# Performance work log

Measured on AMD Instinct MI355X. Metric: run time of the kernel, lower is better.

Reference implementation:

```python
import jax, jax.numpy as jnp
import numpy as np

B, S, L, D = 16, 24, 128, 768
A, T = 8, 8
VOCAB = 100


def setup_inputs() -> dict:
    key = jax.random.key(0)
    k1, k2, k3, k4, k5 = jax.random.split(key, 5)
    return {
        "sentence_embeddings": jax.random.normal(k1, (B, S, L, D), dtype=jnp.float32),
        "sentence_attention_masks": jnp.ones((B, S, L), dtype=jnp.int32),
        "sentence_ids": jax.random.randint(k2, (B, S, L), 0, VOCAB, dtype=jnp.int32),
        "predicate_ids": jax.random.randint(k3, (B, S, A, T), 0, VOCAB, dtype=jnp.int32),
        "arg0_ids": jax.random.randint(k4, (B, S, A, T), 0, VOCAB, dtype=jnp.int32),
        "arg1_ids": jax.random.randint(k5, (B, S, A, T), 0, VOCAB, dtype=jnp.int32),
    }


def _mean_pool(emb, masks):
    # emb: [B,S,L,D], masks: [B,S,L] -> [B,S,D]
    m = masks.astype(emb.dtype)
    summed = jnp.einsum("bsld,bsl->bsd", emb, m)
    counts = jnp.clip(jnp.sum(m, axis=-1, keepdims=True), 1, None)
    return summed / counts


def _arg_embedding(arg_ids, sentence_ids, emb):
    # arg_ids: [B,S,A,T] int, sentence_ids: [B,S,L] int, emb: [B,S,L,D]
    # For each arg token (id != 0), mean-pool sentence positions with matching id.
    # Original loop overwrites per token, so the result is from the LAST nonzero
    # token that has at least one match; zeros if none.
    match = (sentence_ids[:, :, None, None, :] == arg_ids[..., None]) & (
        arg_ids[..., None] != 0
    )  # [B,S,A,T,L]
    m = match.astype(emb.dtype)
    cnt = jnp.sum(m, axis=-1)  # [B,S,A,T]
    avg = jnp.einsum("bsatl,bsld->bsatd", m, emb) / jnp.maximum(cnt, 1.0)[..., None]
    valid = cnt > 0  # nonzero token AND has matches
    t_idx = jnp.arange(arg_ids.shape[-1])
    last = jnp.max(jnp.where(valid, t_idx, -1), axis=-1)  # [B,S,A]
    has_any = last >= 0
    gat = jnp.take_along_axis(
        avg, jnp.maximum(last, 0)[..., None, None], axis=3
    ).squeeze(3)  # [B,S,A,D]
    return jnp.where(has_any[..., None], gat, jnp.zeros((), emb.dtype))


def reference(sentence_embeddings, sentence_attention_masks, sentence_ids,
              predicate_ids, arg0_ids, arg1_ids):
    sentence_embeddings_avg = _mean_pool(sentence_embeddings, sentence_attention_masks)
    predicate_embeddings = _arg_embedding(predicate_ids, sentence_ids, sentence_embeddings)
    arg0_embeddings = _arg_embedding(arg0_ids, sentence_ids, sentence_embeddings)
    arg1_embeddings = _arg_embedding(arg1_ids, sentence_ids, sentence_embeddings)
    return (sentence_embeddings_avg, predicate_embeddings, arg0_embeddings, arg1_embeddings)
```

## Files before the change

### kernel.cpp

```cpp
#include <hip/hip_runtime.h>
#include <cstdint>
#include <cstddef>

#define B_ 16
#define S_ 24
#define L_ 128
#define D_ 768
#define A_ 8
#define T_ 8
#define NSLOT 24
#define HALF_D 384
#define THREADS 192
#define QC 96
#define CHUNK 8

__global__ void __launch_bounds__(THREADS)
srl_kernel(const float* __restrict__ emb,
           const int* __restrict__ masks,
           const int* __restrict__ sids,
           const int* __restrict__ pred,
           const int* __restrict__ arg0,
           const int* __restrict__ arg1,
           float* __restrict__ out)
{
    const int blk  = blockIdx.x;
    const int bs   = blk >> 1;
    const int half = blk & 1;
    const int tid  = threadIdx.x;
    const int r    = tid / QC;
    const int c    = tid % QC;

    __shared__ int          sid_sh[L_];
    __shared__ float        mval_sh[L_];
    __shared__ float        inv_mask_cnt;
    __shared__ int          id_st[NSLOT][T_];
    __shared__ int          cnt_st[NSLOT][T_];
    __shared__ int          chosen_id[NSLOT];
    __shared__ float        inv_cnt[NSLOT];
    __shared__ unsigned int lmask[L_];
    __shared__ float        slot_acc[NSLOT][HALF_D];
    __shared__ float        pool_sh[QC][4];

    if (tid < L_) {
        sid_sh[tid]  = sids[bs * L_ + tid];
        mval_sh[tid] = (float)masks[bs * L_ + tid];
    }
    __syncthreads();

    {
        const int s24 = tid >> 3;
        const int t   = tid & 7;
        const int g   = s24 >> 3;
        const int a   = s24 & 7;
        const int* argp = (g == 0) ? pred : (g == 1) ? arg0 : arg1;
        const int id = argp[((bs * A_) + a) * T_ + t];
        int cnt = 0;
        if (id != 0) {
            #pragma unroll 8
            for (int l = 0; l < L_; ++l) cnt += (sid_sh[l] == id) ? 1 : 0;
        }
        id_st[s24][t]  = id;
        cnt_st[s24][t] = cnt;
    }

    {
        float* p = &slot_acc[0][0];
        for (int i = tid; i < NSLOT * HALF_D; i += THREADS) p[i] = 0.0f;
    }
    if (tid == 0) {
        float cm = 0.0f;
        for (int l = 0; l < L_; ++l) cm += mval_sh[l];
        inv_mask_cnt = 1.0f / fmaxf(cm, 1.0f);
    }
    __syncthreads();

    if (tid < NSLOT) {
        int cid = -1;
        int ccnt = 0;
        for (int t = T_ - 1; t >= 0; --t) {
            if (cnt_st[tid][t] > 0) { cid = id_st[tid][t]; ccnt = cnt_st[tid][t]; break; }
        }
        chosen_id[tid] = cid;
        inv_cnt[tid]   = (ccnt > 0) ? (1.0f / (float)ccnt) : 0.0f;
    }
    __syncthreads();

    if (tid < L_) {
        const int s = sid_sh[tid];
        unsigned int m = 0;
        #pragma unroll
        for (int k = 0; k < NSLOT; ++k)
            m |= (unsigned int)(chosen_id[k] == s) << k;
        lmask[tid] = m;
    }
    __syncthreads();

    const float* rp = emb + (size_t)bs * (L_ * D_) + (size_t)r * D_
                    + half * HALF_D + 4 * c;
    float4 p4 = make_float4(0.f, 0.f, 0.f, 0.f);
    for (int i0 = 0; i0 < L_ / 2; i0 += CHUNK) {
        float4 v[CHUNK];
        #pragma unroll
        for (int j = 0; j < CHUNK; ++j)
            v[j] = *(const float4*)(rp + (size_t)(i0 + j) * (2 * D_));
        #pragma unroll
        for (int j = 0; j < CHUNK; ++j) {
            const int l = r + 2 * (i0 + j);
            const float mk = mval_sh[l];
            p4.x = fmaf(v[j].x, mk, p4.x);
            p4.y = fmaf(v[j].y, mk, p4.y);
            p4.z = fmaf(v[j].z, mk, p4.z);
            p4.w = fmaf(v[j].w, mk, p4.w);
            unsigned int m = lmask[l];
            while (m) {
                const int s24 = __ffs(m) - 1;
                m &= m - 1;
                float* ap = &slot_acc[s24][4 * c];
                atomicAdd(ap + 0, v[j].x);
                atomicAdd(ap + 1, v[j].y);
                atomicAdd(ap + 2, v[j].z);
                atomicAdd(ap + 3, v[j].w);
            }
        }
    }

    if (r == 1) {
        pool_sh[c][0] = p4.x; pool_sh[c][1] = p4.y;
        pool_sh[c][2] = p4.z; pool_sh[c][3] = p4.w;
    }
    __syncthreads();

    const size_t out0_sz = (size_t)B_ * S_ * D_;
    const size_t arg_sz  = (size_t)B_ * S_ * A_ * D_;
    const int d0 = half * HALF_D + 4 * c;

    if (r == 0) {
        float4 o;
        o.x = (p4.x + pool_sh[c][0]) * inv_mask_cnt;
        o.y = (p4.y + pool_sh[c][1]) * inv_mask_cnt;
        o.z = (p4.z + pool_sh[c][2]) * inv_mask_cnt;
        o.w = (p4.w + pool_sh[c][3]) * inv_mask_cnt;
        *(float4*)(out + (size_t)bs * D_ + d0) = o;
    }
    #pragma unroll
    for (int si = 0; si < NSLOT / 2; ++si) {
        const int s24 = r * (NSLOT / 2) + si;
        const int g = s24 >> 3;
        const int a = s24 & 7;
        const float ic = inv_cnt[s24];
        const float* ap = &slot_acc[s24][4 * c];
        float4 o;
        o.x = ap[0] * ic; o.y = ap[1] * ic;
        o.z = ap[2] * ic; o.w = ap[3] * ic;
        float* dst = out + out0_sz + (size_t)g * arg_sz
                   + ((size_t)(bs * A_ + a)) * D_ + d0;
        *(float4*)dst = o;
    }
}

extern "C" void kernel_launch(void* const* d_in, const int* in_sizes, int n_in,
                              void* d_out, int out_size, void* d_ws, size_t ws_size,
                              hipStream_t stream) {
    const float* emb = (const float*)d_in[0];
    const int* masks = (const int*)d_in[1];
    const int* sids  = (const int*)d_in[2];
    const int* pred  = (const int*)d_in[3];
    const int* a0    = (const int*)d_in[4];
    const int* a1    = (const int*)d_in[5];
    float* out = (float*)d_out;

    srl_kernel<<<dim3(2 * B_ * S_), dim3(THREADS), 0, stream>>>(
        emb, masks, sids, pred, a0, a1, out);
}
```

Baseline: 273.4 us.

## Split pooling and per-slot argument gathers into separate block roles

```diff
diff --git a/kernel.cpp b/kernel.cpp
--- a/kernel.cpp
+++ b/kernel.cpp
@@ -13,147 +13,141 @@
 #define THREADS 192
 #define QC 96
 #define CHUNK 8
+#define POOL_BLOCKS (2 * B_ * S_)
+#define ARG_BLOCKS  (NSLOT * B_ * S_)
 
-__global__ void __launch_bounds__(THREADS)
-srl_kernel(const float* __restrict__ emb,
-           const int* __restrict__ masks,
-           const int* __restrict__ sids,
-           const int* __restrict__ pred,
-           const int* __restrict__ arg0,
-           const int* __restrict__ arg1,
-           float* __restrict__ out)
+__global__ void __launch_bounds__(THREADS, 4)
+srl_fused(const float* __restrict__ emb,
+          const int* __restrict__ masks,
+          const int* __restrict__ sids,
+          const int* __restrict__ pred,
+          const int* __restrict__ arg0,
+          const int* __restrict__ arg1,
+          float* __restrict__ out)
 {
-    const int blk  = blockIdx.x;
-    const int bs   = blk >> 1;
-    const int half = blk & 1;
-    const int tid  = threadIdx.x;
-    const int r    = tid / QC;
-    const int c    = tid % QC;
+    const int tid = threadIdx.x;
+    const size_t out0_sz = (size_t)B_ * S_ * D_;
+    const size_t arg_sz  = (size_t)B_ * S_ * A_ * D_;
 
-    __shared__ int          sid_sh[L_];
-    __shared__ float        mval_sh[L_];
-    __shared__ float        inv_mask_cnt;
-    __shared__ int          id_st[NSLOT][T_];
-    __shared__ int          cnt_st[NSLOT][T_];
-    __shared__ int          chosen_id[NSLOT];
-    __shared__ float        inv_cnt[NSLOT];
-    __shared__ unsigned int lmask[L_];
-    __shared__ float        slot_acc[NSLOT][HALF_D];
-    __shared__ float        pool_sh[QC][4];
+    if (blockIdx.x < POOL_BLOCKS) {
+        const int blk  = blockIdx.x;
+        const int bs   = blk >> 1;
+        const int half = blk & 1;
+        const int r    = tid / QC;
+        const int c    = tid % QC;
 
-    if (tid < L_) {
-        sid_sh[tid]  = sids[bs * L_ + tid];
-        mval_sh[tid] = (float)masks[bs * L_ + tid];
-    }
-    __syncthreads();
+        __shared__ float mval_sh[L_];
+        __shared__ float pool_sh[QC][4];
+        __shared__ float inv_sh;
 
-    {
-        const int s24 = tid >> 3;
-        const int t   = tid & 7;
-        const int g   = s24 >> 3;
-        const int a   = s24 & 7;
-        const int* argp = (g == 0) ? pred : (g == 1) ? arg0 : arg1;
-        const int id = argp[((bs * A_) + a) * T_ + t];
-        int cnt = 0;
-        if (id != 0) {
-            #pragma unroll 8
-            for (int l = 0; l < L_; ++l) cnt += (sid_sh[l] == id) ? 1 : 0;
+        if (tid < L_) mval_sh[tid] = (float)masks[bs * L_ + tid];
+        __syncthreads();
+
+        if (tid < 64) {
+            float v = mval_sh[tid] + mval_sh[tid + 64];
+            #pragma unroll
+            for (int off = 32; off; off >>= 1) v += __shfl_down(v, off, 64);
+            if (tid == 0) inv_sh = 1.0f / fmaxf(v, 1.0f);
         }
-        id_st[s24][t]  = id;
-        cnt_st[s24][t] = cnt;
-    }
 
-    {
-        float* p = &slot_acc[0][0];
-        for (int i = tid; i < NSLOT * HALF_D; i += THREADS) p[i] = 0.0f;
-    }
-    if (tid == 0) {
-        float cm = 0.0f;
-        for (int l = 0; l < L_; ++l) cm += mval_sh[l];
-        inv_mask_cnt = 1.0f / fmaxf(cm, 1.0f);
-    }
-    __syncthreads();
-
-    if (tid < NSLOT) {
-        int cid = -1;
-        int ccnt = 0;
-        for (int t = T_ - 1; t >= 0; --t) {
-            if (cnt_st[tid][t] > 0) { cid = id_st[tid][t]; ccnt = cnt_st[tid][t]; break; }
-        }
-        chosen_id[tid] = cid;
-        inv_cnt[tid]   = (ccnt > 0) ? (1.0f / (float)ccnt) : 0.0f;
-    }
-    __syncthreads();
-
-    if (tid < L_) {
-        const int s = sid_sh[tid];
-        unsigned int m = 0;
-        #pragma unroll
-        for (int k = 0; k < NSLOT; ++k)
-            m |= (unsigned int)(chosen_id[k] == s) << k;
-        lmask[tid] = m;
-    }
-    __syncthreads();
-
-    const float* rp = emb + (size_t)bs * (L_ * D_) + (size_t)r * D_
-                    + half * HALF_D + 4 * c;
-    float4 p4 = make_float4(0.f, 0.f, 0.f, 0.f);
-    for (int i0 = 0; i0 < L_ / 2; i0 += CHUNK) {
-        float4 v[CHUNK];
-        #pragma unroll
-        for (int j = 0; j < CHUNK; ++j)
-            v[j] = *(const float4*)(rp + (size_t)(i0 + j) * (2 * D_));
-        #pragma unroll
-        for (int j = 0; j < CHUNK; ++j) {
-            const int l = r + 2 * (i0 + j);
-            const float mk = mval_sh[l];
-            p4.x = fmaf(v[j].x, mk, p4.x);
-            p4.y = fmaf(v[j].y, mk, p4.y);
-            p4.z = fmaf(v[j].z, mk, p4.z);
-            p4.w = fmaf(v[j].w, mk, p4.w);
-            unsigned int m = lmask[l];
-            while (m) {
-                const int s24 = __ffs(m) - 1;
-                m &= m - 1;
-                float* ap = &slot_acc[s24][4 * c];
-                atomicAdd(ap + 0, v[j].x);
-                atomicAdd(ap + 1, v[j].y);
-                atomicAdd(ap + 2, v[j].z);
-                atomicAdd(ap + 3, v[j].w);
+        const float* rp = emb + (size_t)bs * (L_ * D_) + (size_t)r * D_
+                        + half * HALF_D + 4 * c;
+        float4 p = make_float4(0.f, 0.f, 0.f, 0.f);
+        for (int i0 = 0; i0 < L_ / 2; i0 += CHUNK) {
+            float4 v[CHUNK];
+            #pragma unroll
+            for (int j = 0; j < CHUNK; ++j)
+                v[j] = *(const float4*)(rp + (size_t)(i0 + j) * (2 * D_));
+            #pragma unroll
+            for (int j = 0; j < CHUNK; ++j) {
+                const float mk = mval_sh[r + 2 * (i0 + j)];
+                p.x = fmaf(v[j].x, mk, p.x);
+                p.y = fmaf(v[j].y, mk, p.y);
+                p.z = fmaf(v[j].z, mk, p.z);
+                p.w = fmaf(v[j].w, mk, p.w);
             }
         }
-    }
+        if (r == 1) {
+            pool_sh[c][0] = p.x; pool_sh[c][1] = p.y;
+            pool_sh[c][2] = p.z; pool_sh[c][3] = p.w;
+        }
+        __syncthreads();
+        if (r == 0) {
+            const float iv = inv_sh;
+            float4 o;
+            o.x = (p.x + pool_sh[c][0]) * iv;
+            o.y = (p.y + pool_sh[c][1]) * iv;
+            o.z = (p.z + pool_sh[c][2]) * iv;
+            o.w = (p.w + pool_sh[c][3]) * iv;
+            *(float4*)(out + (size_t)bs * D_ + half * HALF_D + 4 * c) = o;
+        }
+    } else {
+        const int task = blockIdx.x - POOL_BLOCKS;
+        const int bs   = task / NSLOT;
+        const int slot = task - bs * NSLOT;
+        const int g    = slot >> 3;
+        const int a    = slot & 7;
 
-    if (r == 1) {
-        pool_sh[c][0] = p4.x; pool_sh[c][1] = p4.y;
-        pool_sh[c][2] = p4.z; pool_sh[c][3] = p4.w;
-    }
-    __syncthreads();
+        __shared__ int   sid_sh[L_];
+        __shared__ int   tok_id[T_];
+        __shared__ int   tok_cnt[T_];
+        __shared__ int   cid_sh;
+        __shared__ float inv_sh2;
+        __shared__ int   mlist[L_];
+        __shared__ int   mcount;
 
-    const size_t out0_sz = (size_t)B_ * S_ * D_;
-    const size_t arg_sz  = (size_t)B_ * S_ * A_ * D_;
-    const int d0 = half * HALF_D + 4 * c;
+        if (tid < L_) sid_sh[tid] = sids[bs * L_ + tid];
+        if (tid < T_) {
+            const int* ap = (g == 0) ? pred : (g == 1) ? arg0 : arg1;
+            tok_id[tid]  = ap[(bs * A_ + a) * T_ + tid];
+            tok_cnt[tid] = 0;
+        }
+        if (tid == 0) mcount = 0;
+        __syncthreads();
 
-    if (r == 0) {
+        for (int idx = tid; idx < T_ * L_; idx += THREADS) {
+            const int t  = idx >> 7;
+            const int l  = idx & (L_ - 1);
+            const int id = tok_id[t];
+            if (id != 0 && sid_sh[l] == id) atomicAdd(&tok_cnt[t], 1);
+        }
+        __syncthreads();
+
+        if (tid == 0) {
+            int cid = -1; float iv = 0.f;
+            for (int t = T_ - 1; t >= 0; --t)
+                if (tok_cnt[t] > 0) { cid = tok_id[t]; iv = 1.0f / (float)tok_cnt[t]; break; }
+            cid_sh = cid; inv_sh2 = iv;
+        }
+        __syncthreads();
+
+        if (tid < L_ && sid_sh[tid] == cid_sh) {
+            const int pos = atomicAdd(&mcount, 1);
+            mlist[pos] = tid;
+        }
+        __syncthreads();
+        if (tid == 0) {
+            const int n = mcount;
+            for (int i = 1; i < n; ++i) {
+                const int key = mlist[i]; int j = i - 1;
+                while (j >= 0 && mlist[j] > key) { mlist[j + 1] = mlist[j]; --j; }
+                mlist[j + 1] = key;
+            }
+        }
+        __syncthreads();
+
+        const int n = mcount;
+        float4 acc = make_float4(0.f, 0.f, 0.f, 0.f);
+        const float* base = emb + (size_t)bs * (L_ * D_) + 4 * tid;
+        for (int i = 0; i < n; ++i) {
+            const float4 v = *(const float4*)(base + (size_t)mlist[i] * D_);
+            acc.x += v.x; acc.y += v.y; acc.z += v.z; acc.w += v.w;
+        }
+        const float iv = inv_sh2;
         float4 o;
-        o.x = (p4.x + pool_sh[c][0]) * inv_mask_cnt;
-        o.y = (p4.y + pool_sh[c][1]) * inv_mask_cnt;
-        o.z = (p4.z + pool_sh[c][2]) * inv_mask_cnt;
-        o.w = (p4.w + pool_sh[c][3]) * inv_mask_cnt;
-        *(float4*)(out + (size_t)bs * D_ + d0) = o;
-    }
-    #pragma unroll
-    for (int si = 0; si < NSLOT / 2; ++si) {
-        const int s24 = r * (NSLOT / 2) + si;
-        const int g = s24 >> 3;
-        const int a = s24 & 7;
-        const float ic = inv_cnt[s24];
-        const float* ap = &slot_acc[s24][4 * c];
-        float4 o;
-        o.x = ap[0] * ic; o.y = ap[1] * ic;
-        o.z = ap[2] * ic; o.w = ap[3] * ic;
+        o.x = acc.x * iv; o.y = acc.y * iv; o.z = acc.z * iv; o.w = acc.w * iv;
         float* dst = out + out0_sz + (size_t)g * arg_sz
-                   + ((size_t)(bs * A_ + a)) * D_ + d0;
+                   + (size_t)(bs * A_ + a) * D_ + 4 * tid;
         *(float4*)dst = o;
     }
 }
@@ -169,6 +163,6 @@
     const int* a1    = (const int*)d_in[5];
     float* out = (float*)d_out;
 
-    srl_kernel<<<dim3(2 * B_ * S_), dim3(THREADS), 0, stream>>>(
+    srl_fused<<<dim3(POOL_BLOCKS + ARG_BLOCKS), dim3(THREADS), 0, stream>>>(
         emb, masks, sids, pred, a0, a1, out);
 }
```

Result: faster. 239.1 us (-12.5%).
